# Kernel optimization log

Measured on AMD Instinct MI355X. Metric: run time of the kernel, lower is better.

## Reference

```python
import jax, jax.numpy as jnp
import numpy as np

N = 50000
E = 800000
DIM = 256
H = 8
D = DIM // H


def setup_inputs() -> dict:
    key = jax.random.key(0)
    ks = jax.random.split(key, 12)
    s = 1.0 / np.sqrt(DIM)
    return {
        "x": jax.random.normal(ks[0], (N, DIM), dtype=jnp.float32),
        "Wq": jax.random.normal(ks[1], (DIM, DIM), dtype=jnp.float32) * s,
        "bq": jax.random.normal(ks[2], (DIM,), dtype=jnp.float32) * 0.01,
        "Wk": jax.random.normal(ks[3], (DIM, DIM), dtype=jnp.float32) * s,
        "bk": jax.random.normal(ks[4], (DIM,), dtype=jnp.float32) * 0.01,
        "Wv": jax.random.normal(ks[5], (DIM, DIM), dtype=jnp.float32) * s,
        "bv": jax.random.normal(ks[6], (DIM,), dtype=jnp.float32) * 0.01,
        "Wo": jax.random.normal(ks[7], (DIM, DIM), dtype=jnp.float32) * s,
        "bo": jax.random.normal(ks[8], (DIM,), dtype=jnp.float32) * 0.01,
        "src": jax.random.randint(ks[9], (E,), 0, N, dtype=jnp.int32),
        "dst": jax.random.randint(ks[10], (E,), 0, N, dtype=jnp.int32),
    }


def reference(x, Wq, bq, Wk, bk, Wv, bv, Wo, bo, src, dst):
    # Linear projections (torch Linear: x @ W.T + b), then [N, H, D]
    q = (x @ Wq.T + bq).reshape(N, H, D)
    k = (x @ Wk.T + bk).reshape(N, H, D)
    v = (x @ Wv.T + bv).reshape(N, H, D)

    # u_dot_v: per-edge dot(queries[src], keys[dst]) -> [E, H]
    scores = jnp.einsum('ehd,ehd->eh', q[src], k[dst]) / jnp.sqrt(jnp.float32(D))

    # edge_softmax over incoming edges of each destination node
    smax = jax.ops.segment_max(scores, dst, num_segments=N)  # [N, H]
    e = jnp.exp(scores - smax[dst])                          # [E, H]
    ssum = jax.ops.segment_sum(e, dst, num_segments=N)       # [N, H]
    probs = e / ssum[dst]                                    # [E, H]

    # u_mul_e_sum: sum over incoming edges of values[src] * probs -> [N, H, D]
    out = jax.ops.segment_sum(v[src] * probs[:, :, None], dst, num_segments=N)

    out = out.reshape(N, DIM)
    return out @ Wo.T + bo  # dropout is identity at p=0 / eval
```

## Files before the change

### kernel.cpp

```cpp
#include <hip/hip_runtime.h>
#include <hip/hip_bf16.h>
#include <math.h>

#define DIMV 256
#define DV 32
#define QKVS 768

typedef __attribute__((ext_vector_type(8))) short bf16x8;
typedef __attribute__((ext_vector_type(4))) float f32x4;

#define EXPS(x) __expf(x)
#define SCORE_SCALE 0.17677669529663687f

static __device__ __forceinline__ unsigned short f2bf(float f) {
    unsigned x = __float_as_uint(f);
    x += 0x7FFF + ((x >> 16) & 1);
    return (unsigned short)(x >> 16);
}
static __device__ __forceinline__ float bf2f(unsigned short u) {
    return __uint_as_float(((unsigned)u) << 16);
}

static __device__ __forceinline__ void async16(const void* g, void* lds) {
    __builtin_amdgcn_global_load_lds(
        (const __attribute__((address_space(1))) void*)g,
        (__attribute__((address_space(3))) void*)lds, 16, 0, 0);
}

static __device__ __forceinline__ void waitvm(int n) {
    switch (n) {
    case 0: asm volatile("s_waitcnt vmcnt(0)" ::: "memory"); break;
    case 2: asm volatile("s_waitcnt vmcnt(2)" ::: "memory"); break;
    default: asm volatile("s_waitcnt vmcnt(4)" ::: "memory"); break;
    }
}


__global__ void cvt_w_count(const float* __restrict__ Wq, const float* __restrict__ Wk,
                            const float* __restrict__ Wv, const float* __restrict__ Wo,
                            unsigned short* __restrict__ Wcat,
                            const int* __restrict__ dst, int* __restrict__ deg, int E) {
    int g = blockIdx.x * 256 + threadIdx.x;
    int m = g >> 13;
    const float* W = m == 0 ? Wq : m == 1 ? Wk : m == 2 ? Wv : Wo;
    int r = g & 8191;
    int h = r >> 12, k = (r >> 9) & 7, f = r & 511;
    int n = f >> 6, kg = (f >> 4) & 3, col = f & 15;
    int c = h * 128 + n * 16 + col;
    int koff = k * 32 + kg * 8;
    const float* src = W + c * 256 + koff;
    float4 f0 = *(const float4*)src;
    float4 f1 = *(const float4*)(src + 4);
    bf16x8 o;
    o[0] = (short)f2bf(f0.x); o[1] = (short)f2bf(f0.y);
    o[2] = (short)f2bf(f0.z); o[3] = (short)f2bf(f0.w);
    o[4] = (short)f2bf(f1.x); o[5] = (short)f2bf(f1.y);
    o[6] = (short)f2bf(f1.z); o[7] = (short)f2bf(f1.w);
    *(bf16x8*)(Wcat + (size_t)g * 8) = o;

    int nthr = gridDim.x * 256;
    for (int e = g; e < E; e += nthr) atomicAdd(&deg[dst[e]], 1);
}


__global__ void zero_i32(int* __restrict__ p, int n) {
    int i = blockIdx.x * blockDim.x + threadIdx.x;
    if (i < n) p[i] = 0;
}

__global__ void block_sum(const int* __restrict__ deg, int* __restrict__ bsum, int n) {
    __shared__ int sm[256];
    int i = blockIdx.x * 256 + threadIdx.x;
    sm[threadIdx.x] = (i < n) ? deg[i] : 0;
    __syncthreads();
    for (int s = 128; s > 0; s >>= 1) {
        if (threadIdx.x < s) sm[threadIdx.x] += sm[threadIdx.x + s];
        __syncthreads();
    }
    if (threadIdx.x == 0) bsum[blockIdx.x] = sm[0];
}

__global__ void scan_bsum(int* __restrict__ bsum, int nb) {
    if (threadIdx.x == 0) {
        int r = 0;
        for (int i = 0; i < nb; ++i) { int v = bsum[i]; bsum[i] = r; r += v; }
    }
}

__global__ void scan_final(const int* __restrict__ deg, const int* __restrict__ bsum,
                           int* __restrict__ offsets, int* __restrict__ cursor, int n) {
    __shared__ int sm[256];
    int i = blockIdx.x * 256 + threadIdx.x;
    int v = (i < n) ? deg[i] : 0;
    sm[threadIdx.x] = v;
    __syncthreads();
    for (int s = 1; s < 256; s <<= 1) {
        int t = (threadIdx.x >= s) ? sm[threadIdx.x - s] : 0;
        __syncthreads();
        sm[threadIdx.x] += t;
        __syncthreads();
    }
    int excl = sm[threadIdx.x] - v + bsum[blockIdx.x];
    if (i < n) { offsets[i] = excl; cursor[i] = excl; }
    if (i == n - 1) offsets[n] = excl + v;
}


template<bool AF32, bool OF32, int NCT, int OSTRIDE, bool SCATTER>
__global__ __launch_bounds__(256)
void gemm_reg(const void* __restrict__ Ain,
              const unsigned short* __restrict__ Wb,
              const float* __restrict__ b0, const float* __restrict__ b1,
              const float* __restrict__ b2,
              void* __restrict__ Cout, int M, int scb,
              const int* __restrict__ esrc, const int* __restrict__ edst,
              int* __restrict__ cursor, int* __restrict__ perm_src, int E) {
    if (SCATTER && (int)blockIdx.x < scb) {
        int nthr = scb * 256;
        for (int e = (int)blockIdx.x * 256 + (int)threadIdx.x; e < E; e += nthr)
            perm_src[atomicAdd(&cursor[edst[e]], 1)] = esrc[e];
        return;
    }
    __shared__ unsigned short Bls[4][4096];
    __shared__ unsigned short Tls[4 * 2176];
    __shared__ float BiasLds[NCT * 128];

    const int bid = (int)blockIdx.x - (SCATTER ? scb : 0);
    const int tid = threadIdx.x, w = tid >> 6, lane = tid & 63;
    const int lrow = lane & 15, lkg = lane >> 4;
    const int row0 = bid * 64;
    const int STOT = NCT * 8;

    for (int i = tid; i < NCT * 128; i += 256) {
        int mat = i >> 8;
        const float* bp = mat == 0 ? b0 : (mat == 1 ? b1 : b2);
        BiasLds[i] = bp[i & 255];
    }

    auto stage = [&](int s) {
        const char* gsrc = (const char*)Wb + (size_t)s * 8192 + w * 2048 + lane * 16;
        #pragma unroll
        for (int j = 0; j < 2; ++j)
            async16(gsrc + j * 1024, (char*)&Bls[s & 3][0] + (w * 2048 + j * 1024));
    };
    stage(0); stage(1); stage(2);

    bf16x8 a[8];
    {
        int arow = min(row0 + w * 16 + lrow, M - 1);
        if (AF32) {
            const float* ap = (const float*)Ain + (size_t)arow * DIMV + lkg * 8;
            #pragma unroll
            for (int k = 0; k < 8; ++k) {
                float4 f0 = *(const float4*)(ap + k * 32);
                float4 f1 = *(const float4*)(ap + k * 32 + 4);
                bf16x8 r;
                r[0] = (short)f2bf(f0.x); r[1] = (short)f2bf(f0.y);
                r[2] = (short)f2bf(f0.z); r[3] = (short)f2bf(f0.w);
                r[4] = (short)f2bf(f1.x); r[5] = (short)f2bf(f1.y);
                r[6] = (short)f2bf(f1.z); r[7] = (short)f2bf(f1.w);
                a[k] = r;
            }
        } else {
            const unsigned short* ap = (const unsigned short*)Ain + (size_t)arow * DIMV + lkg * 8;
            #pragma unroll
            for (int k = 0; k < 8; ++k)
                a[k] = *(const bf16x8*)(ap + k * 32);
        }
    }

    asm volatile("s_waitcnt vmcnt(0) lgkmcnt(0)" ::: "memory");
    __builtin_amdgcn_s_barrier();

    #pragma unroll
    for (int ct = 0; ct < NCT; ++ct) {
        f32x4 acc[8] = {};
        #pragma unroll
        for (int k = 0; k < 8; ++k) {
            const int s = ct * 8 + k;
            if (s == STOT - 1)      waitvm(0);
            else if (s == STOT - 2) waitvm(2);
            else                    waitvm(4);
            __builtin_amdgcn_s_barrier();
            if (s + 3 < STOT) stage(s + 3);
            asm volatile("" ::: "memory");

            const char* base = (const char*)&Bls[s & 3][0];
            bf16x8 bF[8];
            #pragma unroll
            for (int n = 0; n < 8; ++n)
                bF[n] = *(const bf16x8*)(base + n * 1024 + lane * 16);
            asm volatile("s_waitcnt lgkmcnt(0)" ::: "memory");
            __builtin_amdgcn_sched_barrier(0);
            #pragma unroll
            for (int n = 0; n < 8; ++n)
                acc[n] = __builtin_amdgcn_mfma_f32_16x16x32_bf16(a[k], bF[n], acc[n], 0, 0, 0);
        }
        asm volatile("" ::: "memory");

        if (OF32) {
            #pragma unroll
            for (int n = 0; n < 8; ++n) {
                float bias = BiasLds[ct * 128 + n * 16 + lrow];
                #pragma unroll
                for (int r = 0; r < 4; ++r) {
                    int grow = row0 + w * 16 + lkg * 4 + r;
                    if (grow < M)
                        ((float*)Cout)[(size_t)grow * OSTRIDE + ct * 128 + n * 16 + lrow] =
                            acc[n][r] + bias;
                }
            }
        } else {
            #pragma unroll
            for (int n = 0; n < 8; ++n) {
                float bias = BiasLds[ct * 128 + n * 16 + lrow];
                #pragma unroll
                for (int r = 0; r < 4; ++r)
                    Tls[w * 2176 + (lkg * 4 + r) * 136 + n * 16 + lrow] =
                        f2bf(acc[n][r] + bias);
            }
            asm volatile("s_waitcnt lgkmcnt(0)" ::: "memory");
            #pragma unroll
            for (int j = 0; j < 4; ++j) {
                int srow = j * 4 + lkg;
                bf16x8 v = *(const bf16x8*)(&Tls[w * 2176 + srow * 136 + lrow * 8]);
                int grow = row0 + w * 16 + srow;
                if (grow < M)
                    *(bf16x8*)((unsigned short*)Cout + (size_t)grow * OSTRIDE +
                               ct * 128 + lrow * 8) = v;
            }
        }
        asm volatile("" ::: "memory");
    }
}


__global__ __launch_bounds__(256)
void node_attn(const unsigned short* __restrict__ QKV,
               const int* __restrict__ offsets, const int* __restrict__ perm_src,
               unsigned short* __restrict__ attn, int N) {
    int wid = blockIdx.x * (blockDim.x >> 6) + (threadIdx.x >> 6);
    if (wid >= N) return;
    int lane = threadIdx.x & 63;
    unsigned col = (unsigned)((lane >> 3) * DV + (lane & 7) * 4);

    ushort4 kr = *(const ushort4*)(QKV + (size_t)wid * QKVS + 256 + col);
    float k0 = bf2f(kr.x) * SCORE_SCALE, k1 = bf2f(kr.y) * SCORE_SCALE;
    float k2 = bf2f(kr.z) * SCORE_SCALE, k3 = bf2f(kr.w) * SCORE_SCALE;

    float mA = -INFINITY, lA = 0.f, aA0 = 0.f, aA1 = 0.f, aA2 = 0.f, aA3 = 0.f;
    float mB = -INFINITY, lB = 0.f, aB0 = 0.f, aB1 = 0.f, aB2 = 0.f, aB3 = 0.f;

    auto upd = [&](ushort4 qr, ushort4 vr, float& m, float& l,
                   float& a0, float& a1, float& a2, float& a3) {
        float d = bf2f(qr.x) * k0 + bf2f(qr.y) * k1 + bf2f(qr.z) * k2 + bf2f(qr.w) * k3;
        d += __shfl_xor(d, 1); d += __shfl_xor(d, 2); d += __shfl_xor(d, 4);
        float mn = fmaxf(m, d);
        float sc = EXPS(m - mn);
        float pe = EXPS(d - mn);
        l = l * sc + pe;
        a0 = a0 * sc + pe * bf2f(vr.x);
        a1 = a1 * sc + pe * bf2f(vr.y);
        a2 = a2 * sc + pe * bf2f(vr.z);
        a3 = a3 * sc + pe * bf2f(vr.w);
        m = mn;
    };

    int e0 = offsets[wid], e1 = offsets[wid + 1];
    int rem = e1 - e0;
    int S = rem >> 1;
    int p = e0;

    if (S >= 1) {
        unsigned o0 = (unsigned)perm_src[p] * QKVS + col;
        unsigned o1 = (unsigned)perm_src[p + 1] * QKVS + col;
        ushort4 qA0 = *(const ushort4*)(QKV + o0);
        ushort4 vA0 = *(const ushort4*)(QKV + o0 + 512);
        ushort4 qA1 = *(const ushort4*)(QKV + o1);
        ushort4 vA1 = *(const ushort4*)(QKV + o1 + 512);
        unsigned n0 = 0, n1 = 0;
        if (S >= 2) {
            n0 = (unsigned)perm_src[p + 2] * QKVS + col;
            n1 = (unsigned)perm_src[p + 3] * QKVS + col;
        }
        ushort4 qB0, qB1, vB0, vB1;

        int s = 0;
        while (s + 2 <= S) {
            qB0 = *(const ushort4*)(QKV + n0);
            vB0 = *(const ushort4*)(QKV + n0 + 512);
            qB1 = *(const ushort4*)(QKV + n1);
            vB1 = *(const ushort4*)(QKV + n1 + 512);
            if (s + 2 < S) {
                n0 = (unsigned)perm_src[p + 2 * s + 4] * QKVS + col;
                n1 = (unsigned)perm_src[p + 2 * s + 5] * QKVS + col;
            }
            upd(qA0, vA0, mA, lA, aA0, aA1, aA2, aA3);
            upd(qA1, vA1, mB, lB, aB0, aB1, aB2, aB3);

            if (s + 2 < S) {
                qA0 = *(const ushort4*)(QKV + n0);
                vA0 = *(const ushort4*)(QKV + n0 + 512);
                qA1 = *(const ushort4*)(QKV + n1);
                vA1 = *(const ushort4*)(QKV + n1 + 512);
                if (s + 3 < S) {
                    n0 = (unsigned)perm_src[p + 2 * s + 6] * QKVS + col;
                    n1 = (unsigned)perm_src[p + 2 * s + 7] * QKVS + col;
                }
            }
            upd(qB0, vB0, mA, lA, aA0, aA1, aA2, aA3);
            upd(qB1, vB1, mB, lB, aB0, aB1, aB2, aB3);
            s += 2;
        }
        if (s < S) {
            upd(qA0, vA0, mA, lA, aA0, aA1, aA2, aA3);
            upd(qA1, vA1, mB, lB, aB0, aB1, aB2, aB3);
        }
    }
    if (rem & 1) {
        unsigned o0 = (unsigned)perm_src[e1 - 1] * QKVS + col;
        ushort4 q0 = *(const ushort4*)(QKV + o0);
        ushort4 v0 = *(const ushort4*)(QKV + o0 + 512);
        upd(q0, v0, mA, lA, aA0, aA1, aA2, aA3);
    }

    float mn = fmaxf(mA, mB);
    float scA = (lA > 0.f) ? EXPS(mA - mn) : 0.f;
    float scB = (lB > 0.f) ? EXPS(mB - mn) : 0.f;
    float l = lA * scA + lB * scB;
    float o0 = aA0 * scA + aB0 * scB;
    float o1 = aA1 * scA + aB1 * scB;
    float o2 = aA2 * scA + aB2 * scB;
    float o3 = aA3 * scA + aB3 * scB;
    float inv = (l > 0.f) ? 1.f / l : 0.f;

    ushort4 o;
    o.x = f2bf(o0 * inv); o.y = f2bf(o1 * inv); o.z = f2bf(o2 * inv); o.w = f2bf(o3 * inv);
    *(ushort4*)(attn + (size_t)wid * DIMV + col) = o;
}


extern "C" void kernel_launch(void* const* d_in, const int* in_sizes, int n_in,
                              void* d_out, int out_size, void* d_ws, size_t ws_size,
                              hipStream_t stream) {
    const float* x  = (const float*)d_in[0];
    const float* Wq = (const float*)d_in[1];
    const float* bq = (const float*)d_in[2];
    const float* Wk = (const float*)d_in[3];
    const float* bk = (const float*)d_in[4];
    const float* Wv = (const float*)d_in[5];
    const float* bv = (const float*)d_in[6];
    const float* Wo = (const float*)d_in[7];
    const float* bo = (const float*)d_in[8];
    const int* src  = (const int*)d_in[9];
    const int* dst  = (const int*)d_in[10];
    int N = in_sizes[0] / DIMV;
    int E = in_sizes[9];
    float* out = (float*)d_out;

    char* p = (char*)d_ws;
    auto alloc = [&](size_t bytes) {
        char* r = p;
        p += (bytes + 255) & ~(size_t)255;
        return r;
    };
    unsigned short* Wcat = (unsigned short*)alloc((size_t)4 * 65536 * 2);
    unsigned short* QKV  = (unsigned short*)alloc((size_t)N * QKVS * 2);
    unsigned short* attn = (unsigned short*)alloc((size_t)N * DIMV * 2);
    int* deg             = (int*)alloc((size_t)N * 4);
    int* offsets         = (int*)alloc((size_t)(N + 1) * 4);
    int* cursor          = (int*)alloc((size_t)N * 4);
    int* perm_src        = (int*)alloc((size_t)E * 4);
    int* bsum            = (int*)alloc((size_t)1024 * 4);

    int nb = (N + 255) / 256;
    zero_i32<<<nb, 256, 0, stream>>>(deg, N);

    cvt_w_count<<<128, 256, 0, stream>>>(Wq, Wk, Wv, Wo, Wcat, dst, deg, E);

    block_sum<<<nb, 256, 0, stream>>>(deg, bsum, N);
    scan_bsum<<<1, 64, 0, stream>>>(bsum, nb);
    scan_final<<<nb, 256, 0, stream>>>(deg, bsum, offsets, cursor, N);

    int rblocks = (N + 63) / 64;
    const int SCB = 160;
    gemm_reg<true, false, 6, QKVS, true><<<SCB + rblocks, 256, 0, stream>>>(
        x, Wcat, bq, bk, bv, QKV, N, SCB, src, dst, cursor, perm_src, E);

    node_attn<<<(N + 3) / 4, 256, 0, stream>>>(QKV, offsets, perm_src, attn, N);

    gemm_reg<false, true, 2, DIMV, false><<<rblocks, 256, 0, stream>>>(
        attn, Wcat + (size_t)3 * 65536, bo, bo, bo, out, N, 0,
        nullptr, nullptr, nullptr, nullptr, 0);
}
```

Before: 269.3 us.

## Stream weight fragments from global into registers with a 2x2 warp tiling in GEMMs

The GEMM kernel no longer stages weights through LDS with async loads and block barriers. Each wave now loads its own 64-column weight fragments straight from global (L2-resident) into a 3-deep register ring, and computes a 32x64 tile in a 2x2 wave layout, so each B fragment feeds two MFMAs. Bias is read directly from global instead of LDS. This removes the per-k-step barriers and LDS traffic, but raises register pressure (two A row-sets held) and doubles global weight reads per block, since each wave pair loads the same columns.

```diff
diff --git a/kernel.cpp b/kernel.cpp
--- a/kernel.cpp
+++ b/kernel.cpp
@@ -19,20 +19,6 @@
 }
 static __device__ __forceinline__ float bf2f(unsigned short u) {
     return __uint_as_float(((unsigned)u) << 16);
-}
-
-static __device__ __forceinline__ void async16(const void* g, void* lds) {
-    __builtin_amdgcn_global_load_lds(
-        (const __attribute__((address_space(1))) void*)g,
-        (__attribute__((address_space(3))) void*)lds, 16, 0, 0);
-}
-
-static __device__ __forceinline__ void waitvm(int n) {
-    switch (n) {
-    case 0: asm volatile("s_waitcnt vmcnt(0)" ::: "memory"); break;
-    case 2: asm volatile("s_waitcnt vmcnt(2)" ::: "memory"); break;
-    default: asm volatile("s_waitcnt vmcnt(4)" ::: "memory"); break;
-    }
 }
 
 
@@ -108,46 +94,32 @@
 
 template<bool AF32, bool OF32, int NCT, int OSTRIDE, bool SCATTER>
 __global__ __launch_bounds__(256)
-void gemm_reg(const void* __restrict__ Ain,
-              const unsigned short* __restrict__ Wb,
-              const float* __restrict__ b0, const float* __restrict__ b1,
-              const float* __restrict__ b2,
-              void* __restrict__ Cout, int M, int scb,
-              const int* __restrict__ esrc, const int* __restrict__ edst,
-              int* __restrict__ cursor, int* __restrict__ perm_src, int E) {
+void gemm_stream(const void* __restrict__ Ain,
+                 const unsigned short* __restrict__ Wb,
+                 const float* __restrict__ b0, const float* __restrict__ b1,
+                 const float* __restrict__ b2,
+                 void* __restrict__ Cout, int M, int scb,
+                 const int* __restrict__ esrc, const int* __restrict__ edst,
+                 int* __restrict__ cursor, int* __restrict__ perm_src, int E) {
     if (SCATTER && (int)blockIdx.x < scb) {
         int nthr = scb * 256;
         for (int e = (int)blockIdx.x * 256 + (int)threadIdx.x; e < E; e += nthr)
             perm_src[atomicAdd(&cursor[edst[e]], 1)] = esrc[e];
         return;
     }
-    __shared__ unsigned short Bls[4][4096];
-    __shared__ unsigned short Tls[4 * 2176];
-    __shared__ float BiasLds[NCT * 128];
+    __shared__ unsigned short Tls[4][32][68];
 
     const int bid = (int)blockIdx.x - (SCATTER ? scb : 0);
     const int tid = threadIdx.x, w = tid >> 6, lane = tid & 63;
+    const int wr = w >> 1, wc = w & 1;
     const int lrow = lane & 15, lkg = lane >> 4;
     const int row0 = bid * 64;
     const int STOT = NCT * 8;
 
-    for (int i = tid; i < NCT * 128; i += 256) {
-        int mat = i >> 8;
-        const float* bp = mat == 0 ? b0 : (mat == 1 ? b1 : b2);
-        BiasLds[i] = bp[i & 255];
-    }
-
-    auto stage = [&](int s) {
-        const char* gsrc = (const char*)Wb + (size_t)s * 8192 + w * 2048 + lane * 16;
-        #pragma unroll
-        for (int j = 0; j < 2; ++j)
-            async16(gsrc + j * 1024, (char*)&Bls[s & 3][0] + (w * 2048 + j * 1024));
-    };
-    stage(0); stage(1); stage(2);
-
-    bf16x8 a[8];
-    {
-        int arow = min(row0 + w * 16 + lrow, M - 1);
+    bf16x8 a[2][8];
+    #pragma unroll
+    for (int m = 0; m < 2; ++m) {
+        int arow = min(row0 + wr * 32 + m * 16 + lrow, M - 1);
         if (AF32) {
             const float* ap = (const float*)Ain + (size_t)arow * DIMV + lkg * 8;
             #pragma unroll
@@ -159,78 +131,85 @@
                 r[2] = (short)f2bf(f0.z); r[3] = (short)f2bf(f0.w);
                 r[4] = (short)f2bf(f1.x); r[5] = (short)f2bf(f1.y);
                 r[6] = (short)f2bf(f1.z); r[7] = (short)f2bf(f1.w);
-                a[k] = r;
+                a[m][k] = r;
             }
         } else {
             const unsigned short* ap = (const unsigned short*)Ain + (size_t)arow * DIMV + lkg * 8;
             #pragma unroll
             for (int k = 0; k < 8; ++k)
-                a[k] = *(const bf16x8*)(ap + k * 32);
-        }
-    }
-
-    asm volatile("s_waitcnt vmcnt(0) lgkmcnt(0)" ::: "memory");
-    __builtin_amdgcn_s_barrier();
+                a[m][k] = *(const bf16x8*)(ap + k * 32);
+        }
+    }
+
+    const char* wbase = (const char*)Wb + (size_t)(wc * 4) * 1024 + (size_t)lane * 16;
+
+    bf16x8 b[3][4];
+    #pragma unroll
+    for (int j = 0; j < 3; ++j) {
+        const char* p = wbase + (size_t)j * 8192;
+        #pragma unroll
+        for (int n = 0; n < 4; ++n)
+            b[j][n] = *(const bf16x8*)(p + n * 1024);
+    }
 
     #pragma unroll
     for (int ct = 0; ct < NCT; ++ct) {
-        f32x4 acc[8] = {};
+        f32x4 acc[2][4] = {};
         #pragma unroll
         for (int k = 0; k < 8; ++k) {
             const int s = ct * 8 + k;
-            if (s == STOT - 1)      waitvm(0);
-            else if (s == STOT - 2) waitvm(2);
-            else                    waitvm(4);
-            __builtin_amdgcn_s_barrier();
-            if (s + 3 < STOT) stage(s + 3);
-            asm volatile("" ::: "memory");
-
-            const char* base = (const char*)&Bls[s & 3][0];
-            bf16x8 bF[8];
-            #pragma unroll
-            for (int n = 0; n < 8; ++n)
-                bF[n] = *(const bf16x8*)(base + n * 1024 + lane * 16);
+            #pragma unroll
+            for (int n = 0; n < 4; ++n) {
+                acc[0][n] = __builtin_amdgcn_mfma_f32_16x16x32_bf16(a[0][k], b[s % 3][n], acc[0][n], 0, 0, 0);
+                acc[1][n] = __builtin_amdgcn_mfma_f32_16x16x32_bf16(a[1][k], b[s % 3][n], acc[1][n], 0, 0, 0);
+            }
+            if (s + 3 < STOT) {
+                const char* p = wbase + (size_t)(s + 3) * 8192;
+                #pragma unroll
+                for (int n = 0; n < 4; ++n)
+                    b[s % 3][n] = *(const bf16x8*)(p + n * 1024);
+            }
+        }
+
+        if (OF32) {
+            #pragma unroll
+            for (int n = 0; n < 4; ++n) {
+                int c = ct * 128 + wc * 64 + n * 16 + lrow;
+                const float* bp = (c >> 8) == 0 ? b0 : ((c >> 8) == 1 ? b1 : b2);
+                float bias = bp[c & 255];
+                #pragma unroll
+                for (int m = 0; m < 2; ++m)
+                    #pragma unroll
+                    for (int r = 0; r < 4; ++r) {
+                        int grow = row0 + wr * 32 + m * 16 + lkg * 4 + r;
+                        if (grow < M)
+                            ((float*)Cout)[(size_t)grow * OSTRIDE + c] = acc[m][n][r] + bias;
+                    }
+            }
+        } else {
+            #pragma unroll
+            for (int n = 0; n < 4; ++n) {
+                int c = ct * 128 + wc * 64 + n * 16 + lrow;
+                const float* bp = (c >> 8) == 0 ? b0 : ((c >> 8) == 1 ? b1 : b2);
+                float bias = bp[c & 255];
+                #pragma unroll
+                for (int m = 0; m < 2; ++m)
+                    #pragma unroll
+                    for (int r = 0; r < 4; ++r)
+                        Tls[w][m * 16 + lkg * 4 + r][n * 16 + lrow] = f2bf(acc[m][n][r] + bias);
+            }
             asm volatile("s_waitcnt lgkmcnt(0)" ::: "memory");
-            __builtin_amdgcn_sched_barrier(0);
-            #pragma unroll
-            for (int n = 0; n < 8; ++n)
-                acc[n] = __builtin_amdgcn_mfma_f32_16x16x32_bf16(a[k], bF[n], acc[n], 0, 0, 0);
-        }
-        asm volatile("" ::: "memory");
-
-        if (OF32) {
-            #pragma unroll
-            for (int n = 0; n < 8; ++n) {
-                float bias = BiasLds[ct * 128 + n * 16 + lrow];
-                #pragma unroll
-                for (int r = 0; r < 4; ++r) {
-                    int grow = row0 + w * 16 + lkg * 4 + r;
-                    if (grow < M)
-                        ((float*)Cout)[(size_t)grow * OSTRIDE + ct * 128 + n * 16 + lrow] =
-                            acc[n][r] + bias;
-                }
-            }
-        } else {
-            #pragma unroll
-            for (int n = 0; n < 8; ++n) {
-                float bias = BiasLds[ct * 128 + n * 16 + lrow];
-                #pragma unroll
-                for (int r = 0; r < 4; ++r)
-                    Tls[w * 2176 + (lkg * 4 + r) * 136 + n * 16 + lrow] =
-                        f2bf(acc[n][r] + bias);
-            }
-            asm volatile("s_waitcnt lgkmcnt(0)" ::: "memory");
             #pragma unroll
             for (int j = 0; j < 4; ++j) {
-                int srow = j * 4 + lkg;
-                bf16x8 v = *(const bf16x8*)(&Tls[w * 2176 + srow * 136 + lrow * 8]);
-                int grow = row0 + w * 16 + srow;
+                int rloc = j * 8 + (lane >> 3);
+                bf16x8 v = *(const bf16x8*)(&Tls[w][rloc][(lane & 7) * 8]);
+                int grow = row0 + wr * 32 + rloc;
                 if (grow < M)
                     *(bf16x8*)((unsigned short*)Cout + (size_t)grow * OSTRIDE +
-                               ct * 128 + lrow * 8) = v;
-            }
-        }
-        asm volatile("" ::: "memory");
+                               ct * 128 + wc * 64 + (lane & 7) * 8) = v;
+            }
+            asm volatile("s_waitcnt lgkmcnt(0)" ::: "memory");
+        }
     }
 }
 
@@ -384,12 +363,12 @@
 
     int rblocks = (N + 63) / 64;
     const int SCB = 160;
-    gemm_reg<true, false, 6, QKVS, true><<<SCB + rblocks, 256, 0, stream>>>(
+    gemm_stream<true, false, 6, QKVS, true><<<SCB + rblocks, 256, 0, stream>>>(
         x, Wcat, bq, bk, bv, QKV, N, SCB, src, dst, cursor, perm_src, E);
 
     node_attn<<<(N + 3) / 4, 256, 0, stream>>>(QKV, offsets, perm_src, attn, N);
 
-    gemm_reg<false, true, 2, DIMV, false><<<rblocks, 256, 0, stream>>>(
+    gemm_stream<false, true, 2, DIMV, false><<<rblocks, 256, 0, stream>>>(
         attn, Wcat + (size_t)3 * 65536, bo, bo, bo, out, N, 0,
         nullptr, nullptr, nullptr, nullptr, 0);
 }
```

After: 289.8 us. 7.6% more time.
